# Optimization experiments

Hardware: AMD Instinct MI355X
Metric: run time of the kernel (lower is better)

The kernel has to match this reference:

```python
import jax, jax.numpy as jnp
import numpy as np

N_NODES = 50000
N_EDGES = 800000
F = 64
R = 32


def setup_inputs() -> dict:
    key = jax.random.key(0)
    ks = jax.random.split(key, 12)
    s = jax.random.normal(ks[0], (N_NODES, F), dtype=jnp.float32)
    v = jax.random.normal(ks[1], (N_NODES, 3, F), dtype=jnp.float32)
    radial_embeddings = jax.random.normal(ks[2], (N_EDGES, R), dtype=jnp.float32)
    f_cut = jax.random.uniform(ks[3], (N_EDGES,), dtype=jnp.float32)
    unit_vectors = jax.random.normal(ks[4], (N_EDGES, 3), dtype=jnp.float32)
    edge_index = jax.random.randint(ks[5], (2, N_EDGES), 0, N_NODES, dtype=jnp.int64 if jax.config.jax_enable_x64 else jnp.int32)
    # mlp_phi: Linear(F,F) -> SiLU -> Linear(F, 3F); linear_W: Linear(R, 3F)
    W1 = jax.random.normal(ks[6], (F, F), dtype=jnp.float32) / np.sqrt(F)
    b1 = jnp.zeros((F,), dtype=jnp.float32)
    W2 = jax.random.normal(ks[7], (F, 3 * F), dtype=jnp.float32) / np.sqrt(F)
    b2 = jnp.zeros((3 * F,), dtype=jnp.float32)
    Wr = jax.random.normal(ks[8], (R, 3 * F), dtype=jnp.float32) / np.sqrt(R)
    br = jnp.zeros((3 * F,), dtype=jnp.float32)
    return {"s": s, "v": v, "radial_embeddings": radial_embeddings, "f_cut": f_cut,
            "unit_vectors": unit_vectors, "edge_index": edge_index,
            "W1": W1, "b1": b1, "W2": W2, "b2": b2, "Wr": Wr, "br": br}


def reference(s, v, radial_embeddings, f_cut, unit_vectors, edge_index, W1, b1, W2, b2, Wr, br):
    idx_i, idx_j = edge_index[0], edge_index[1]
    n_nodes = s.shape[0]
    nf = s.shape[-1]
    # per-node MLP: Linear -> SiLU -> Linear to 3F channels
    phi = jax.nn.silu(s @ W1 + b1) @ W2 + b2            # [N, 3F]
    # radial filter weighted by cutoff
    W = (radial_embeddings @ Wr + br) * f_cut[:, None]   # [E, 3F]
    x = phi[idx_j] * W                                   # [E, 3F]  (gather + multiply)
    x_s, x_vv, x_vs = x[:, :nf], x[:, nf:2 * nf], x[:, 2 * nf:]
    ds = jax.ops.segment_sum(x_s, idx_i, num_segments=n_nodes)          # [N, F]
    x_v = v[idx_j] * x_vv[:, None, :] + x_vs[:, None, :] * unit_vectors[:, :, None]  # [E, 3, F]
    dv = jax.ops.segment_sum(x_v, idx_i, num_segments=n_nodes)          # [N, 3, F]
    return s + ds, v + dv
```

## Files before the change

### kernel.cpp

```cpp
#include <hip/hip_runtime.h>
#include <math.h>

#define N_NODES 50000
#define N_EDGES 800000
#define F 64
#define R 32
#define C3F 192
#define CAP 48
#define CSTRIDE 16
#define MLP_BLOCKS ((N_NODES + 31) / 32)
#define FILL_BLOCKS ((N_EDGES + 255) / 256)

#define REP32(X) X(0) X(1) X(2) X(3) X(4) X(5) X(6) X(7) \
                 X(8) X(9) X(10) X(11) X(12) X(13) X(14) X(15) \
                 X(16) X(17) X(18) X(19) X(20) X(21) X(22) X(23) \
                 X(24) X(25) X(26) X(27) X(28) X(29) X(30) X(31)

__global__ __launch_bounds__(256) void mlp_fill_kernel(
    const float* __restrict__ s, const float* __restrict__ W1,
    const float* __restrict__ b1, const float* __restrict__ W2,
    const float* __restrict__ b2, float* __restrict__ phi,
    const int* __restrict__ eidx, int* __restrict__ counts,
    int2* __restrict__ bucket)
{
    __shared__ float hid_s[32][68];

    if (blockIdx.x >= MLP_BLOCKS) {
        int e = (blockIdx.x - MLP_BLOCKS) * 256 + threadIdx.x;
        if (e < N_EDGES) {
            int i = eidx[e];
            int j = eidx[N_EDGES + e];
            int pos = atomicAdd(&counts[i * CSTRIDE], 1);
            if (pos < CAP) bucket[(size_t)i * CAP + pos] = make_int2(e, j);
        }
        return;
    }

    int n = threadIdx.x >> 3;
    int seg = threadIdx.x & 7;
    int node = blockIdx.x * 32 + n;
    bool live = node < N_NODES;

    if (live) {
        float sv[F];
        const float4* srow = (const float4*)(s + (size_t)node * F);
#pragma unroll
        for (int q = 0; q < F / 4; q++) {
            float4 t = srow[q];
            sv[4*q+0] = t.x; sv[4*q+1] = t.y; sv[4*q+2] = t.z; sv[4*q+3] = t.w;
        }
        float acc[8];
#pragma unroll
        for (int q = 0; q < 8; q++) acc[q] = b1[seg * 8 + q];
#pragma unroll
        for (int k = 0; k < F; k++) {
            float sk = sv[k];
            const float4* w = (const float4*)(W1 + (size_t)k * F + seg * 8);
            float4 w0 = w[0], w1 = w[1];
            acc[0] += sk * w0.x; acc[1] += sk * w0.y;
            acc[2] += sk * w0.z; acc[3] += sk * w0.w;
            acc[4] += sk * w1.x; acc[5] += sk * w1.y;
            acc[6] += sk * w1.z; acc[7] += sk * w1.w;
        }
#pragma unroll
        for (int q = 0; q < 8; q++) {
            float a = acc[q];
            hid_s[n][seg * 8 + q] = a / (1.f + __expf(-a));
        }
    }
    __syncthreads();

    if (!live) return;

    float hv[F];
#pragma unroll
    for (int q = 0; q < F; q++) hv[q] = hid_s[n][q];

    float acc[24];
#pragma unroll
    for (int q = 0; q < 24; q++) acc[q] = b2[seg * 24 + q];
#pragma unroll
    for (int k = 0; k < F; k++) {
        float hk = hv[k];
        const float4* w = (const float4*)(W2 + (size_t)k * C3F + seg * 24);
#pragma unroll
        for (int q4 = 0; q4 < 6; q4++) {
            float4 wv = w[q4];
            acc[q4*4+0] += hk * wv.x;
            acc[q4*4+1] += hk * wv.y;
            acc[q4*4+2] += hk * wv.z;
            acc[q4*4+3] += hk * wv.w;
        }
    }
    float4* o = (float4*)(phi + (size_t)node * C3F + seg * 24);
#pragma unroll
    for (int q4 = 0; q4 < 6; q4++)
        o[q4] = make_float4(acc[q4*4+0], acc[q4*4+1], acc[q4*4+2], acc[q4*4+3]);
}

__global__ __launch_bounds__(64, 4) void gather_kernel(
    const float* __restrict__ s, const float* __restrict__ v,
    const float* __restrict__ phi, const float* __restrict__ radial,
    const float* __restrict__ f_cut, const float* __restrict__ unit_vec,
    const float* __restrict__ Wr, const float* __restrict__ br,
    const int* __restrict__ counts, const int2* __restrict__ bucket,
    float* __restrict__ out_s, float* __restrict__ out_v)
{
    const int lane = threadIdx.x;
    const int node = blockIdx.x;

#define DECL_WR(r) float wrs##r, wrv##r, wrq##r;
    REP32(DECL_WR)
#undef DECL_WR
#define LOAD_WR(r) { const float* w_ = Wr + (r) * C3F; \
                     wrs##r = w_[lane]; wrv##r = w_[64 + lane]; \
                     wrq##r = w_[128 + lane]; }
    REP32(LOAD_WR)
#undef LOAD_WR
#define KA3(r) , "+v"(wrs##r), "+v"(wrv##r), "+v"(wrq##r)
    asm volatile("" : "+v"(wrs0) KA3(1) KA3(2) KA3(3) KA3(4) KA3(5) KA3(6) KA3(7), "+v"(wrv0), "+v"(wrq0));
    asm volatile("" : "+v"(wrs8) KA3(9) KA3(10) KA3(11) KA3(12) KA3(13) KA3(14) KA3(15), "+v"(wrv8), "+v"(wrq8));
    asm volatile("" : "+v"(wrs16) KA3(17) KA3(18) KA3(19) KA3(20) KA3(21) KA3(22) KA3(23), "+v"(wrv16), "+v"(wrq16));
    asm volatile("" : "+v"(wrs24) KA3(25) KA3(26) KA3(27) KA3(28) KA3(29) KA3(30) KA3(31), "+v"(wrv24), "+v"(wrq24));
#undef KA3

    const float b_s = br[lane], b_vv = br[64 + lane], b_vs = br[128 + lane];

    float acc_s = 0.f, acc_v0 = 0.f, acc_v1 = 0.f, acc_v2 = 0.f;

    int cnt = __builtin_amdgcn_readfirstlane(counts[node * CSTRIDE]);
    cnt = cnt < CAP ? cnt : CAP;
    const int2* row = bucket + (size_t)node * CAP;

    if (cnt > 0) {
        int2 ej0 = row[0];
        int e = __builtin_amdgcn_readfirstlane(ej0.x);
        int j = __builtin_amdgcn_readfirstlane(ej0.y);

        const float* pj = phi + (size_t)j * C3F;
        const float* vj = v + (size_t)j * C3F;
        float ps = pj[lane], pvv = pj[64 + lane], pvs = pj[128 + lane];
        float va = vj[lane], vb = vj[64 + lane], vc = vj[128 + lane];

        float fc = f_cut[e];
        float u0 = unit_vec[e * 3 + 0];
        float u1 = unit_vec[e * 3 + 1];
        float u2 = unit_vec[e * 3 + 2];
#define DECL_CR(r) float cr##r;
        REP32(DECL_CR)
#undef DECL_CR
        {
            const float* rp = radial + (size_t)e * R;
#define LOAD_CR(r) cr##r = rp[r];
            REP32(LOAD_CR)
#undef LOAD_CR
        }

        for (int k = 0; k < cnt; ++k) {
            int e_n = e, j_n = j;
            if (k + 1 < cnt) {
                int2 ejn = row[k + 1];
                e_n = __builtin_amdgcn_readfirstlane(ejn.x);
                j_n = __builtin_amdgcn_readfirstlane(ejn.y);
            }
            const float* pn = phi + (size_t)j_n * C3F;
            const float* vn = v + (size_t)j_n * C3F;
            float nps = pn[lane], npvv = pn[64 + lane], npvs = pn[128 + lane];
            float nva = vn[lane], nvb = vn[64 + lane], nvc = vn[128 + lane];
            float fc_n = f_cut[e_n];
            float nu0 = unit_vec[e_n * 3 + 0];
            float nu1 = unit_vec[e_n * 3 + 1];
            float nu2 = unit_vec[e_n * 3 + 2];
#define DECL_NR(r) float nr##r;
            REP32(DECL_NR)
#undef DECL_NR
            {
                const float* rpn = radial + (size_t)e_n * R;
#define LOAD_NR(r) nr##r = rpn[r];
                REP32(LOAD_NR)
#undef LOAD_NR
            }

            float ws = b_s, wvv = b_vv, wvs = b_vs;
#define FMA_WR(r) { ws  += cr##r * wrs##r; \
                    wvv += cr##r * wrv##r; \
                    wvs += cr##r * wrq##r; }
            REP32(FMA_WR)
#undef FMA_WR

            float xs  = ps  * ws  * fc;
            float xvv = pvv * wvv * fc;
            float xvs = pvs * wvs * fc;
            acc_s  += xs;
            acc_v0 += va * xvv + xvs * u0;
            acc_v1 += vb * xvv + xvs * u1;
            acc_v2 += vc * xvv + xvs * u2;

            e = e_n; j = j_n;
            ps = nps; pvv = npvv; pvs = npvs;
            va = nva; vb = nvb; vc = nvc;
            fc = fc_n; u0 = nu0; u1 = nu1; u2 = nu2;
#define ROT_R(r) cr##r = nr##r;
            REP32(ROT_R)
#undef ROT_R
        }
    }

    out_s[(size_t)node * F + lane] = s[(size_t)node * F + lane] + acc_s;
    const float* vi = v + (size_t)node * C3F;
    float* ovi = out_v + (size_t)node * C3F;
    ovi[lane]       = vi[lane]       + acc_v0;
    ovi[64 + lane]  = vi[64 + lane]  + acc_v1;
    ovi[128 + lane] = vi[128 + lane] + acc_v2;
}

extern "C" void kernel_launch(void* const* d_in, const int* in_sizes, int n_in,
                              void* d_out, int out_size, void* d_ws, size_t ws_size,
                              hipStream_t stream)
{
    const float* s      = (const float*)d_in[0];
    const float* v      = (const float*)d_in[1];
    const float* radial = (const float*)d_in[2];
    const float* f_cut  = (const float*)d_in[3];
    const float* unit   = (const float*)d_in[4];
    const int*   eidx   = (const int*)  d_in[5];
    const float* W1     = (const float*)d_in[6];
    const float* b1     = (const float*)d_in[7];
    const float* W2     = (const float*)d_in[8];
    const float* b2     = (const float*)d_in[9];
    const float* Wr     = (const float*)d_in[10];
    const float* br     = (const float*)d_in[11];

    float* out   = (float*)d_out;
    float* out_s = out;
    float* out_v = out + (size_t)N_NODES * F;

    float* phi    = (float*)d_ws;
    int*   counts = (int*)(phi + (size_t)N_NODES * C3F);
    int2*  bucket = (int2*)(counts + (size_t)N_NODES * CSTRIDE);

    hipMemsetAsync(counts, 0, (size_t)N_NODES * CSTRIDE * sizeof(int), stream);

    mlp_fill_kernel<<<MLP_BLOCKS + FILL_BLOCKS, 256, 0, stream>>>(
        s, W1, b1, W2, b2, phi, eidx, counts, bucket);

    gather_kernel<<<N_NODES, 64, 0, stream>>>(
        s, v, phi, radial, f_cut, unit, Wr, br,
        counts, bucket, out_s, out_v);
}
```

Measured before the change: 572.3 us.

## Load radial rows via scalar loads, preload per-edge scalars across lanes, split fill kernel

The gather loop now loads each edge's 32 radial floats with two s_load_dwordx16 scalar loads into SGPRs, double-buffered A/B, instead of 32 per-lane vector loads of uniform data. Edge ids, f_cut and unit vectors for up to 64 edges are loaded once, one per lane, and broadcast with readlane instead of being reloaded every iteration. The fused MLP/fill launch is split into two separate kernels. This cuts vector memory traffic and VGPR pressure, but it depends on hand-written inline asm with a manual lgkmcnt wait and adds one kernel launch.

```diff
diff --git a/kernel.cpp b/kernel.cpp
--- a/kernel.cpp
+++ b/kernel.cpp
@@ -16,25 +16,19 @@
                  X(16) X(17) X(18) X(19) X(20) X(21) X(22) X(23) \
                  X(24) X(25) X(26) X(27) X(28) X(29) X(30) X(31)
 
-__global__ __launch_bounds__(256) void mlp_fill_kernel(
+typedef __attribute__((ext_vector_type(16))) float f32x16;
+
+__device__ __forceinline__ float bcastf(float x, int l) {
+    return __uint_as_float((unsigned)__builtin_amdgcn_readlane(
+        (int)__float_as_uint(x), l));
+}
+
+__global__ __launch_bounds__(256) void mlp_kernel(
     const float* __restrict__ s, const float* __restrict__ W1,
     const float* __restrict__ b1, const float* __restrict__ W2,
-    const float* __restrict__ b2, float* __restrict__ phi,
-    const int* __restrict__ eidx, int* __restrict__ counts,
-    int2* __restrict__ bucket)
+    const float* __restrict__ b2, float* __restrict__ phi)
 {
     __shared__ float hid_s[32][68];
-
-    if (blockIdx.x >= MLP_BLOCKS) {
-        int e = (blockIdx.x - MLP_BLOCKS) * 256 + threadIdx.x;
-        if (e < N_EDGES) {
-            int i = eidx[e];
-            int j = eidx[N_EDGES + e];
-            int pos = atomicAdd(&counts[i * CSTRIDE], 1);
-            if (pos < CAP) bucket[(size_t)i * CAP + pos] = make_int2(e, j);
-        }
-        return;
-    }
 
     int n = threadIdx.x >> 3;
     int seg = threadIdx.x & 7;
@@ -97,6 +91,67 @@
     for (int q4 = 0; q4 < 6; q4++)
         o[q4] = make_float4(acc[q4*4+0], acc[q4*4+1], acc[q4*4+2], acc[q4*4+3]);
 }
+
+__global__ __launch_bounds__(256) void fill_kernel(
+    const int* __restrict__ eidx, int* __restrict__ counts,
+    int2* __restrict__ bucket)
+{
+    int e = blockIdx.x * 256 + threadIdx.x;
+    if (e < N_EDGES) {
+        int i = eidx[e];
+        int j = eidx[N_EDGES + e];
+        int pos = atomicAdd(&counts[i * CSTRIDE], 1);
+        if (pos < CAP) bucket[(size_t)i * CAP + pos] = make_int2(e, j);
+    }
+}
+
+
+#define RAD_LOAD(SET, RP)                                                    \
+    asm volatile("s_load_dwordx16 %0, %2, 0\n\t"                             \
+                 "s_load_dwordx16 %1, %2, 64"                                \
+                 : "=s"(ra##SET##0), "=s"(ra##SET##1)                        \
+                 : "s"(RP))
+
+#define RAD_WAIT(SET)                                                        \
+    asm volatile("s_waitcnt lgkmcnt(0)"                                      \
+                 : "+s"(ra##SET##0), "+s"(ra##SET##1))
+
+#define FMA_WR_A(r) { const float rr = (r) < 16 ? raA0[(r)&15] : raA1[(r)&15]; \
+                      ws += rr * wrs##r; wvv += rr * wrv##r; wvs += rr * wrq##r; }
+#define FMA_WR_B(r) { const float rr = (r) < 16 ? raB0[(r)&15] : raB1[(r)&15]; \
+                      ws += rr * wrs##r; wvv += rr * wrv##r; wvs += rr * wrq##r; }
+#define FMA_ALL_A REP32(FMA_WR_A)
+#define FMA_ALL_B REP32(FMA_WR_B)
+
+#define BODY(CUR, NXT, k)                                                    \
+    {                                                                        \
+        int kn = ((k) + 1 < cnt) ? (k) + 1 : (k);                            \
+        bool pf = kn != (k);                                                 \
+        int e_n = __builtin_amdgcn_readlane(ejx, kn);                        \
+        int j_n = __builtin_amdgcn_readlane(ejy, kn);                        \
+        RAD_WAIT(CUR);                                                       \
+        if (pf) {                                                            \
+            const float* rp_n = radial + (size_t)(unsigned)e_n * R;          \
+            RAD_LOAD(NXT, rp_n);                                             \
+            const float* pn = phi + (size_t)(unsigned)j_n * C3F;             \
+            const float* vn = v + (size_t)(unsigned)j_n * C3F;               \
+            ps##NXT = pn[lane]; pvv##NXT = pn[64 + lane]; pvs##NXT = pn[128 + lane]; \
+            va##NXT = vn[lane]; vb##NXT = vn[64 + lane]; vc##NXT = vn[128 + lane];   \
+        }                                                                    \
+        float fc = bcastf(fcL, (k));                                         \
+        float u0 = bcastf(u0L, (k));                                         \
+        float u1 = bcastf(u1L, (k));                                         \
+        float u2 = bcastf(u2L, (k));                                         \
+        float ws = b_s, wvv = b_vv, wvs = b_vs;                              \
+        FMA_ALL_##CUR;                                                       \
+        float xs  = ps##CUR * ws * fc;                                       \
+        float xvv = pvv##CUR * wvv * fc;                                     \
+        float xvs = pvs##CUR * wvs * fc;                                     \
+        acc_s  += xs;                                                        \
+        acc_v0 += va##CUR * xvv + xvs * u0;                                  \
+        acc_v1 += vb##CUR * xvv + xvs * u1;                                  \
+        acc_v2 += vc##CUR * xvv + xvs * u2;                                  \
+    }
 
 __global__ __launch_bounds__(64, 4) void gather_kernel(
     const float* __restrict__ s, const float* __restrict__ v,
@@ -132,77 +187,33 @@
     cnt = cnt < CAP ? cnt : CAP;
     const int2* row = bucket + (size_t)node * CAP;
 
+    int2 ejv = make_int2(0, 0);
+    if (lane < cnt) ejv = row[lane];
+    int ejx = ejv.x, ejy = ejv.y;
+    float fcL = f_cut[ejx];
+    float u0L = unit_vec[ejx * 3 + 0];
+    float u1L = unit_vec[ejx * 3 + 1];
+    float u2L = unit_vec[ejx * 3 + 2];
+
+    f32x16 raA0, raA1, raB0, raB1;
+    float psA = 0.f, pvvA = 0.f, pvsA = 0.f, vaA = 0.f, vbA = 0.f, vcA = 0.f;
+    float psB = 0.f, pvvB = 0.f, pvsB = 0.f, vaB = 0.f, vbB = 0.f, vcB = 0.f;
+
     if (cnt > 0) {
-        int2 ej0 = row[0];
-        int e = __builtin_amdgcn_readfirstlane(ej0.x);
-        int j = __builtin_amdgcn_readfirstlane(ej0.y);
-
-        const float* pj = phi + (size_t)j * C3F;
-        const float* vj = v + (size_t)j * C3F;
-        float ps = pj[lane], pvv = pj[64 + lane], pvs = pj[128 + lane];
-        float va = vj[lane], vb = vj[64 + lane], vc = vj[128 + lane];
-
-        float fc = f_cut[e];
-        float u0 = unit_vec[e * 3 + 0];
-        float u1 = unit_vec[e * 3 + 1];
-        float u2 = unit_vec[e * 3 + 2];
-#define DECL_CR(r) float cr##r;
-        REP32(DECL_CR)
-#undef DECL_CR
+        int e0 = __builtin_amdgcn_readlane(ejx, 0);
+        int j0 = __builtin_amdgcn_readlane(ejy, 0);
         {
-            const float* rp = radial + (size_t)e * R;
-#define LOAD_CR(r) cr##r = rp[r];
-            REP32(LOAD_CR)
-#undef LOAD_CR
-        }
-
-        for (int k = 0; k < cnt; ++k) {
-            int e_n = e, j_n = j;
-            if (k + 1 < cnt) {
-                int2 ejn = row[k + 1];
-                e_n = __builtin_amdgcn_readfirstlane(ejn.x);
-                j_n = __builtin_amdgcn_readfirstlane(ejn.y);
-            }
-            const float* pn = phi + (size_t)j_n * C3F;
-            const float* vn = v + (size_t)j_n * C3F;
-            float nps = pn[lane], npvv = pn[64 + lane], npvs = pn[128 + lane];
-            float nva = vn[lane], nvb = vn[64 + lane], nvc = vn[128 + lane];
-            float fc_n = f_cut[e_n];
-            float nu0 = unit_vec[e_n * 3 + 0];
-            float nu1 = unit_vec[e_n * 3 + 1];
-            float nu2 = unit_vec[e_n * 3 + 2];
-#define DECL_NR(r) float nr##r;
-            REP32(DECL_NR)
-#undef DECL_NR
-            {
-                const float* rpn = radial + (size_t)e_n * R;
-#define LOAD_NR(r) nr##r = rpn[r];
-                REP32(LOAD_NR)
-#undef LOAD_NR
-            }
-
-            float ws = b_s, wvv = b_vv, wvs = b_vs;
-#define FMA_WR(r) { ws  += cr##r * wrs##r; \
-                    wvv += cr##r * wrv##r; \
-                    wvs += cr##r * wrq##r; }
-            REP32(FMA_WR)
-#undef FMA_WR
-
-            float xs  = ps  * ws  * fc;
-            float xvv = pvv * wvv * fc;
-            float xvs = pvs * wvs * fc;
-            acc_s  += xs;
-            acc_v0 += va * xvv + xvs * u0;
-            acc_v1 += vb * xvv + xvs * u1;
-            acc_v2 += vc * xvv + xvs * u2;
-
-            e = e_n; j = j_n;
-            ps = nps; pvv = npvv; pvs = npvs;
-            va = nva; vb = nvb; vc = nvc;
-            fc = fc_n; u0 = nu0; u1 = nu1; u2 = nu2;
-#define ROT_R(r) cr##r = nr##r;
-            REP32(ROT_R)
-#undef ROT_R
+            const float* rp0 = radial + (size_t)(unsigned)e0 * R;
+            RAD_LOAD(A, rp0);
+            const float* p0 = phi + (size_t)(unsigned)j0 * C3F;
+            const float* v0 = v + (size_t)(unsigned)j0 * C3F;
+            psA = p0[lane]; pvvA = p0[64 + lane]; pvsA = p0[128 + lane];
+            vaA = v0[lane]; vbA = v0[64 + lane]; vcA = v0[128 + lane];
+        }
+        int k = 0;
+        while (true) {
+            BODY(A, B, k); ++k; if (k >= cnt) break;
+            BODY(B, A, k); ++k; if (k >= cnt) break;
         }
     }
 
@@ -241,8 +252,9 @@
 
     hipMemsetAsync(counts, 0, (size_t)N_NODES * CSTRIDE * sizeof(int), stream);
 
-    mlp_fill_kernel<<<MLP_BLOCKS + FILL_BLOCKS, 256, 0, stream>>>(
-        s, W1, b1, W2, b2, phi, eidx, counts, bucket);
+    mlp_kernel<<<MLP_BLOCKS, 256, 0, stream>>>(s, W1, b1, W2, b2, phi);
+
+    fill_kernel<<<FILL_BLOCKS, 256, 0, stream>>>(eidx, counts, bucket);
 
     gather_kernel<<<N_NODES, 64, 0, stream>>>(
         s, v, phi, radial, f_cut, unit, Wr, br,
```

Result: slower. 788.2 us (+37.7%).

## Split MLP and fill kernels, keep MLP weights in registers, split gather launch

Applied to the files above, without the earlier changes.

The fused MLP/fill kernel becomes two kernels. The new fill kernel batches four edges per thread with nontemporal index loads. The new MLP kernel is a persistent grid that holds a column of W1 and W2 in registers per lane and processes one node per loop iteration, streaming phi out with nontemporal stores. The gather launch is split into two half-grids with a node offset. This removes repeated weight reads from memory but adds a kernel launch and serialises fill and MLP work that previously ran concurrently.

```diff
diff --git a/kernel.cpp b/kernel.cpp
--- a/kernel.cpp
+++ b/kernel.cpp
@@ -8,94 +8,122 @@
 #define C3F 192
 #define CAP 48
 #define CSTRIDE 16
-#define MLP_BLOCKS ((N_NODES + 31) / 32)
-#define FILL_BLOCKS ((N_EDGES + 255) / 256)
+#define FILL_BLOCKS ((N_EDGES + 1023) / 1024)
+#define MLP_GRID 1024
 
 #define REP32(X) X(0) X(1) X(2) X(3) X(4) X(5) X(6) X(7) \
                  X(8) X(9) X(10) X(11) X(12) X(13) X(14) X(15) \
                  X(16) X(17) X(18) X(19) X(20) X(21) X(22) X(23) \
                  X(24) X(25) X(26) X(27) X(28) X(29) X(30) X(31)
 
-__global__ __launch_bounds__(256) void mlp_fill_kernel(
+#define REP64(X) REP32(X) \
+                 X(32) X(33) X(34) X(35) X(36) X(37) X(38) X(39) \
+                 X(40) X(41) X(42) X(43) X(44) X(45) X(46) X(47) \
+                 X(48) X(49) X(50) X(51) X(52) X(53) X(54) X(55) \
+                 X(56) X(57) X(58) X(59) X(60) X(61) X(62) X(63)
+
+__global__ __launch_bounds__(192, 2) void mlp_kernel(
     const float* __restrict__ s, const float* __restrict__ W1,
     const float* __restrict__ b1, const float* __restrict__ W2,
-    const float* __restrict__ b2, float* __restrict__ phi,
+    const float* __restrict__ b2, float* __restrict__ phi)
+{
+    const int lane = threadIdx.x & 63;
+    const int w    = threadIdx.x >> 6;
+
+    __shared__ float hls[3][64];
+
+#define DECL_W(r) float w1_##r, w2_##r;
+    REP64(DECL_W)
+#undef DECL_W
+#define LOAD_W(r) { w1_##r = W1[(r) * F + lane]; \
+                    w2_##r = W2[(r) * C3F + w * 64 + lane]; }
+    REP64(LOAD_W)
+#undef LOAD_W
+
+#define KW1(r) , "+v"(w1_##r)
+#define KW2(r) , "+v"(w2_##r)
+#define PIN_W \
+    asm volatile("" : "+v"(w1_0) KW1(1) KW1(2) KW1(3) KW1(4) KW1(5) KW1(6) KW1(7) KW1(8) KW1(9) KW1(10) KW1(11) KW1(12) KW1(13) KW1(14) KW1(15)); \
+    asm volatile("" : "+v"(w1_16) KW1(17) KW1(18) KW1(19) KW1(20) KW1(21) KW1(22) KW1(23) KW1(24) KW1(25) KW1(26) KW1(27) KW1(28) KW1(29) KW1(30) KW1(31)); \
+    asm volatile("" : "+v"(w1_32) KW1(33) KW1(34) KW1(35) KW1(36) KW1(37) KW1(38) KW1(39) KW1(40) KW1(41) KW1(42) KW1(43) KW1(44) KW1(45) KW1(46) KW1(47)); \
+    asm volatile("" : "+v"(w1_48) KW1(49) KW1(50) KW1(51) KW1(52) KW1(53) KW1(54) KW1(55) KW1(56) KW1(57) KW1(58) KW1(59) KW1(60) KW1(61) KW1(62) KW1(63)); \
+    asm volatile("" : "+v"(w2_0) KW2(1) KW2(2) KW2(3) KW2(4) KW2(5) KW2(6) KW2(7) KW2(8) KW2(9) KW2(10) KW2(11) KW2(12) KW2(13) KW2(14) KW2(15)); \
+    asm volatile("" : "+v"(w2_16) KW2(17) KW2(18) KW2(19) KW2(20) KW2(21) KW2(22) KW2(23) KW2(24) KW2(25) KW2(26) KW2(27) KW2(28) KW2(29) KW2(30) KW2(31)); \
+    asm volatile("" : "+v"(w2_32) KW2(33) KW2(34) KW2(35) KW2(36) KW2(37) KW2(38) KW2(39) KW2(40) KW2(41) KW2(42) KW2(43) KW2(44) KW2(45) KW2(46) KW2(47)); \
+    asm volatile("" : "+v"(w2_48) KW2(49) KW2(50) KW2(51) KW2(52) KW2(53) KW2(54) KW2(55) KW2(56) KW2(57) KW2(58) KW2(59) KW2(60) KW2(61) KW2(62) KW2(63));
+    PIN_W
+
+    const float b1l = b1[lane];
+    const float b2l = b2[w * 64 + lane];
+
+    for (int node = blockIdx.x; node < N_NODES; node += gridDim.x) {
+        PIN_W
+
+        const float4* sp4 = (const float4*)(s + (size_t)node * F);
+
+        float hh0 = b1l, hh1 = 0.f, hh2 = 0.f, hh3 = 0.f;
+#define HF4(q, r0, r1, r2, r3) { float4 sq = sp4[q]; \
+        hh0 += sq.x * w1_##r0; hh1 += sq.y * w1_##r1; \
+        hh2 += sq.z * w1_##r2; hh3 += sq.w * w1_##r3; }
+        HF4(0, 0, 1, 2, 3)     HF4(1, 4, 5, 6, 7)
+        HF4(2, 8, 9, 10, 11)   HF4(3, 12, 13, 14, 15)
+        HF4(4, 16, 17, 18, 19) HF4(5, 20, 21, 22, 23)
+        HF4(6, 24, 25, 26, 27) HF4(7, 28, 29, 30, 31)
+        HF4(8, 32, 33, 34, 35) HF4(9, 36, 37, 38, 39)
+        HF4(10, 40, 41, 42, 43) HF4(11, 44, 45, 46, 47)
+        HF4(12, 48, 49, 50, 51) HF4(13, 52, 53, 54, 55)
+        HF4(14, 56, 57, 58, 59) HF4(15, 60, 61, 62, 63)
+#undef HF4
+        float a = (hh0 + hh1) + (hh2 + hh3);
+        float hval = a / (1.f + __expf(-a));
+        hls[w][lane] = hval;
+
+        float p0 = b2l, p1 = 0.f, p2 = 0.f, p3 = 0.f;
+        const float4* hp = (const float4*)&hls[w][0];
+#define PF4(q, r0, r1, r2, r3) { float4 hq = hp[q]; \
+        p0 += hq.x * w2_##r0; p1 += hq.y * w2_##r1; \
+        p2 += hq.z * w2_##r2; p3 += hq.w * w2_##r3; }
+        PF4(0, 0, 1, 2, 3)     PF4(1, 4, 5, 6, 7)
+        PF4(2, 8, 9, 10, 11)   PF4(3, 12, 13, 14, 15)
+        PF4(4, 16, 17, 18, 19) PF4(5, 20, 21, 22, 23)
+        PF4(6, 24, 25, 26, 27) PF4(7, 28, 29, 30, 31)
+        PF4(8, 32, 33, 34, 35) PF4(9, 36, 37, 38, 39)
+        PF4(10, 40, 41, 42, 43) PF4(11, 44, 45, 46, 47)
+        PF4(12, 48, 49, 50, 51) PF4(13, 52, 53, 54, 55)
+        PF4(14, 56, 57, 58, 59) PF4(15, 60, 61, 62, 63)
+#undef PF4
+        float pv = (p0 + p1) + (p2 + p3);
+        __builtin_nontemporal_store(pv, &phi[(size_t)node * C3F + w * 64 + lane]);
+    }
+#undef KW1
+#undef KW2
+#undef PIN_W
+}
+
+__global__ __launch_bounds__(256) void fill_kernel(
     const int* __restrict__ eidx, int* __restrict__ counts,
     int2* __restrict__ bucket)
 {
-    __shared__ float hid_s[32][68];
-
-    if (blockIdx.x >= MLP_BLOCKS) {
-        int e = (blockIdx.x - MLP_BLOCKS) * 256 + threadIdx.x;
+    int base = blockIdx.x * 1024 + threadIdx.x;
+    int ii[4], jj[4];
+#pragma unroll
+    for (int q = 0; q < 4; q++) {
+        int e = base + q * 256;
+        ii[q] = -1;
         if (e < N_EDGES) {
-            int i = eidx[e];
-            int j = eidx[N_EDGES + e];
-            int pos = atomicAdd(&counts[i * CSTRIDE], 1);
-            if (pos < CAP) bucket[(size_t)i * CAP + pos] = make_int2(e, j);
-        }
-        return;
-    }
-
-    int n = threadIdx.x >> 3;
-    int seg = threadIdx.x & 7;
-    int node = blockIdx.x * 32 + n;
-    bool live = node < N_NODES;
-
-    if (live) {
-        float sv[F];
-        const float4* srow = (const float4*)(s + (size_t)node * F);
+            ii[q] = __builtin_nontemporal_load(&eidx[e]);
+            jj[q] = __builtin_nontemporal_load(&eidx[N_EDGES + e]);
+        }
+    }
 #pragma unroll
-        for (int q = 0; q < F / 4; q++) {
-            float4 t = srow[q];
-            sv[4*q+0] = t.x; sv[4*q+1] = t.y; sv[4*q+2] = t.z; sv[4*q+3] = t.w;
-        }
-        float acc[8];
-#pragma unroll
-        for (int q = 0; q < 8; q++) acc[q] = b1[seg * 8 + q];
-#pragma unroll
-        for (int k = 0; k < F; k++) {
-            float sk = sv[k];
-            const float4* w = (const float4*)(W1 + (size_t)k * F + seg * 8);
-            float4 w0 = w[0], w1 = w[1];
-            acc[0] += sk * w0.x; acc[1] += sk * w0.y;
-            acc[2] += sk * w0.z; acc[3] += sk * w0.w;
-            acc[4] += sk * w1.x; acc[5] += sk * w1.y;
-            acc[6] += sk * w1.z; acc[7] += sk * w1.w;
-        }
-#pragma unroll
-        for (int q = 0; q < 8; q++) {
-            float a = acc[q];
-            hid_s[n][seg * 8 + q] = a / (1.f + __expf(-a));
-        }
-    }
-    __syncthreads();
-
-    if (!live) return;
-
-    float hv[F];
-#pragma unroll
-    for (int q = 0; q < F; q++) hv[q] = hid_s[n][q];
-
-    float acc[24];
-#pragma unroll
-    for (int q = 0; q < 24; q++) acc[q] = b2[seg * 24 + q];
-#pragma unroll
-    for (int k = 0; k < F; k++) {
-        float hk = hv[k];
-        const float4* w = (const float4*)(W2 + (size_t)k * C3F + seg * 24);
-#pragma unroll
-        for (int q4 = 0; q4 < 6; q4++) {
-            float4 wv = w[q4];
-            acc[q4*4+0] += hk * wv.x;
-            acc[q4*4+1] += hk * wv.y;
-            acc[q4*4+2] += hk * wv.z;
-            acc[q4*4+3] += hk * wv.w;
-        }
-    }
-    float4* o = (float4*)(phi + (size_t)node * C3F + seg * 24);
-#pragma unroll
-    for (int q4 = 0; q4 < 6; q4++)
-        o[q4] = make_float4(acc[q4*4+0], acc[q4*4+1], acc[q4*4+2], acc[q4*4+3]);
+    for (int q = 0; q < 4; q++) {
+        int e = base + q * 256;
+        if (ii[q] >= 0) {
+            int pos = atomicAdd(&counts[ii[q] * CSTRIDE], 1);
+            if (pos < CAP)
+                bucket[(size_t)ii[q] * CAP + pos] = make_int2(e, jj[q]);
+        }
+    }
 }
 
 __global__ __launch_bounds__(64, 4) void gather_kernel(
@@ -104,10 +132,10 @@
     const float* __restrict__ f_cut, const float* __restrict__ unit_vec,
     const float* __restrict__ Wr, const float* __restrict__ br,
     const int* __restrict__ counts, const int2* __restrict__ bucket,
-    float* __restrict__ out_s, float* __restrict__ out_v)
+    float* __restrict__ out_s, float* __restrict__ out_v, int node_base)
 {
     const int lane = threadIdx.x;
-    const int node = blockIdx.x;
+    const int node = node_base + blockIdx.x;
 
 #define DECL_WR(r) float wrs##r, wrv##r, wrq##r;
     REP32(DECL_WR)
@@ -241,10 +269,14 @@
 
     hipMemsetAsync(counts, 0, (size_t)N_NODES * CSTRIDE * sizeof(int), stream);
 
-    mlp_fill_kernel<<<MLP_BLOCKS + FILL_BLOCKS, 256, 0, stream>>>(
-        s, W1, b1, W2, b2, phi, eidx, counts, bucket);
-
-    gather_kernel<<<N_NODES, 64, 0, stream>>>(
+    fill_kernel<<<FILL_BLOCKS, 256, 0, stream>>>(eidx, counts, bucket);
+
+    mlp_kernel<<<MLP_GRID, 192, 0, stream>>>(s, W1, b1, W2, b2, phi);
+
+    gather_kernel<<<N_NODES / 2, 64, 0, stream>>>(
         s, v, phi, radial, f_cut, unit, Wr, br,
-        counts, bucket, out_s, out_v);
-}
+        counts, bucket, out_s, out_v, 0);
+    gather_kernel<<<N_NODES / 2, 64, 0, stream>>>(
+        s, v, phi, radial, f_cut, unit, Wr, br,
+        counts, bucket, out_s, out_v, N_NODES / 2);
+}
```

After: 655.2 us. 1.14x slower.
